# Optimization experiments

Hardware: AMD Instinct MI355X
Metric: run time of the kernel (lower is better)

Reference implementation:

```python
import jax, jax.numpy as jnp
import numpy as np

OUT = 7  # output_size of the ROI pool

def setup_inputs() -> dict:
    key = jax.random.key(0)
    # batched ROI crops: [N_rois, C, H, W] with H=W=14 (divisible by OUT=7,
    # so adaptive max-pool windows are exact non-overlapping 2x2 blocks)
    rois = jax.random.normal(key, (512, 256, 14, 14), dtype=jnp.float32)
    return {"rois": rois}

def reference(rois) -> jnp.ndarray:
    N, C, H, W = rois.shape
    kh, kw = H // OUT, W // OUT
    # AdaptiveMaxPool2d with H % OUT == 0 and W % OUT == 0 reduces to
    # max over non-overlapping (kh, kw) windows: start=floor(i*H/O)=i*kh,
    # end=ceil((i+1)*H/O)=(i+1)*kh, identical to the adaptive formula.
    x = rois.reshape(N, C, OUT, kh, OUT, kw)
    return x.max(axis=(3, 5))  # [N, C, OUT, OUT]
```

## Files before the change

### kernel.cpp

```cpp
#include <hip/hip_runtime.h>


__global__ void ROIPooling_86466281603470_kernel(const float* __restrict__ in,
                                                 float* __restrict__ out,
                                                 int n_out) {
    int idx = blockIdx.x * blockDim.x + threadIdx.x;
    int stride = gridDim.x * blockDim.x;
    for (; idx < n_out; idx += stride) {
        int plane = idx / 49;
        int rem   = idx - plane * 49;
        int i     = rem / 7;
        int j     = rem - i * 7;
        const float* base = in + (size_t)plane * 196 + i * 28;
        float2 a = *reinterpret_cast<const float2*>(base + 2 * j);
        float2 b = *reinterpret_cast<const float2*>(base + 14 + 2 * j);
        out[idx] = fmaxf(fmaxf(a.x, a.y), fmaxf(b.x, b.y));
    }
}

extern "C" void kernel_launch(void* const* d_in, const int* in_sizes, int n_in,
                              void* d_out, int out_size, void* d_ws, size_t ws_size,
                              hipStream_t stream) {
    const float* in = (const float*)d_in[0];
    float* out = (float*)d_out;
    int n_out = out_size;
    int block = 256;
    int grid = (n_out + block - 1) / block;
    if (grid > 2048) grid = 2048;
    ROIPooling_86466281603470_kernel<<<grid, block, 0, stream>>>(in, out, n_out);
}
```

Before: 26.38 us.

## Stage 16 planes per block through LDS with coalesced float4 loads

Each block now copies 16 contiguous 14x14 planes into shared memory with fully coalesced float4 loads, then computes the 2x2 max from LDS and writes outputs contiguously. This replaces strided float2 global loads and the grid-stride loop, aiming at better global memory coalescing and more blocks in flight (8192 blocks). It drops bounds checks, so it assumes the plane count is divisible by 16, and it adds a barrier and 12.5KB of LDS per block.

```diff
diff --git a/kernel.cpp b/kernel.cpp
--- a/kernel.cpp
+++ b/kernel.cpp
@@ -1,20 +1,36 @@
 #include <hip/hip_runtime.h>
 
 
-__global__ void ROIPooling_86466281603470_kernel(const float* __restrict__ in,
-                                                 float* __restrict__ out,
-                                                 int n_out) {
-    int idx = blockIdx.x * blockDim.x + threadIdx.x;
-    int stride = gridDim.x * blockDim.x;
-    for (; idx < n_out; idx += stride) {
-        int plane = idx / 49;
-        int rem   = idx - plane * 49;
-        int i     = rem / 7;
-        int j     = rem - i * 7;
-        const float* base = in + (size_t)plane * 196 + i * 28;
+#define PPB   16
+#define BLOCK 256
+
+__global__ __launch_bounds__(BLOCK)
+void ROIPooling_86466281603470_kernel(const float* __restrict__ in,
+                                      float* __restrict__ out) {
+    __shared__ float lds[PPB * 196];
+
+    const int pb = blockIdx.x * PPB;
+
+    const float4* __restrict__ in4 =
+        reinterpret_cast<const float4*>(in + (size_t)pb * 196);
+    float4* lds4 = reinterpret_cast<float4*>(lds);
+    #pragma unroll
+    for (int v = threadIdx.x; v < PPB * 49; v += BLOCK) {
+        lds4[v] = in4[v];
+    }
+    __syncthreads();
+
+    float* __restrict__ outb = out + (size_t)pb * 49;
+    #pragma unroll
+    for (int o = threadIdx.x; o < PPB * 49; o += BLOCK) {
+        int p   = o / 49;
+        int rem = o - p * 49;
+        int i   = rem / 7;
+        int j   = rem - i * 7;
+        const float* base = lds + p * 196 + i * 28;
         float2 a = *reinterpret_cast<const float2*>(base + 2 * j);
         float2 b = *reinterpret_cast<const float2*>(base + 14 + 2 * j);
-        out[idx] = fmaxf(fmaxf(a.x, a.y), fmaxf(b.x, b.y));
+        outb[o] = fmaxf(fmaxf(a.x, a.y), fmaxf(b.x, b.y));
     }
 }
 
@@ -23,9 +39,7 @@
                               hipStream_t stream) {
     const float* in = (const float*)d_in[0];
     float* out = (float*)d_out;
-    int n_out = out_size;
-    int block = 256;
-    int grid = (n_out + block - 1) / block;
-    if (grid > 2048) grid = 2048;
-    ROIPooling_86466281603470_kernel<<<grid, block, 0, stream>>>(in, out, n_out);
+    int n_planes = out_size / 49;
+    int grid = n_planes / PPB;
+    ROIPooling_86466281603470_kernel<<<grid, BLOCK, 0, stream>>>(in, out);
 }
```

After: 24.72 us. 1.07x faster.
